# Kernel tuning notes

Hardware: AMD Instinct MI355X
Metric: run time of the kernel (lower is better)

## Reference

```python
import jax, jax.numpy as jnp
import numpy as np

D = 6            # tree depth: 63 nodes per tree, leaves-first level order
HL = 256         # lstm hidden dim
HM = 128         # mlp hid dim
OFFSETS = [0, 32, 48, 56, 60, 62]  # level l occupies [off, off+2**(D-1-l))


def _lin(k, fan_in, fan_out, scale=0.02):
    return jax.random.normal(k, (fan_in, fan_out), jnp.float32) * scale


def setup_inputs() -> dict:
    key = jax.random.key(0)
    ks = jax.random.split(key, 40)
    B, N = 1024, 63
    inp = {
        "op": jax.random.normal(ks[0], (B, N, 32), jnp.float32),
        "feat": jax.random.normal(ks[1], (B, N, 64), jnp.float32),
        "cond1": jax.random.normal(ks[2], (B, N, 256), jnp.float32),
        "cond2": jax.random.normal(ks[3], (B, N, 256), jnp.float32),
        "bitmap": jax.random.uniform(ks[4], (B, N, 1000), jnp.float32),
        "has_cond": jnp.ones((B, N), jnp.float32),
        # embeddings (stored [in, out], i.e. transposed torch Linear weight)
        "W_op": _lin(ks[5], 32, HM), "b_op": jnp.zeros((HM,), jnp.float32),
        "W_feat": _lin(ks[6], 64, HM), "b_feat": jnp.zeros((HM,), jnp.float32),
        "W_pred": _lin(ks[7], 256, HM), "b_pred": jnp.zeros((HM,), jnp.float32),
        "W_bm": _lin(ks[8], 1000, HM), "b_bm": jnp.zeros((HM,), jnp.float32),
        # node LSTM (torch layout: [4*HL, in])
        "W_ih": jax.random.normal(ks[9], (4 * HL, 5 * HM), jnp.float32) * 0.02,
        "b_ih": jnp.zeros((4 * HL,), jnp.float32),
        "W_hh": jax.random.normal(ks[10], (4 * HL, HL), jnp.float32) * 0.02,
        "b_hh": jnp.zeros((4 * HL,), jnp.float32),
        # descendant attention
        "W_wh": _lin(ks[11], HL, 64), "W_ext": _lin(ks[12], 5 * HM, 64),
        "W_a": _lin(ks[13], 64, 1),
        "W_ht": _lin(ks[14], HL, HL), "b_ht": jnp.zeros((HL,), jnp.float32),
        # output heads
        "W_c1": _lin(ks[15], HL, HM), "b_c1": jnp.zeros((HM,), jnp.float32),
        "W_c2": _lin(ks[16], HM, HM), "b_c2": jnp.zeros((HM,), jnp.float32),
        "W_c3": _lin(ks[17], HM, 1), "b_c3": jnp.zeros((1,), jnp.float32),
        "W_d1": _lin(ks[18], HL, HM), "b_d1": jnp.zeros((HM,), jnp.float32),
        "W_d2": _lin(ks[19], HM, HM), "b_d2": jnp.zeros((HM,), jnp.float32),
        "W_d3": _lin(ks[20], HM, 1), "b_d3": jnp.zeros((1,), jnp.float32),
    }
    return inp


def _tree_forward(op, feat, cond1, cond2, bitmap, has_cond,
                  W_op, b_op, W_feat, b_feat, W_pred, b_pred, W_bm, b_bm,
                  W_ih, b_ih, W_hh, b_hh, W_wh, W_ext, W_a, W_ht, b_ht):
    B = op.shape[0]
    # per-node 5*HM input vector (conditions are single Compare predicates)
    x = jnp.concatenate([
        op @ W_op + b_op,
        feat @ W_feat + b_feat,
        cond1 @ W_pred + b_pred,
        cond2 @ W_pred + b_pred,
        (bitmap @ W_bm + b_bm) * has_cond[..., None],
    ], axis=-1)                                        # [B, 63, 5*HM]

    hiddens, cells = [], []
    for l in range(D):
        n, off = 2 ** (D - 1 - l), OFFSETS[l]
        xl = x[:, off:off + n]                         # [B, n, 5*HM]
        if l == 0:  # leaves: no children, no descendants
            h0 = jnp.zeros((B, n, HL), x.dtype)
            c0 = h0
        else:
            # all descendant hiddens of each node, grouped per parent
            desc = jnp.concatenate(
                [hiddens[lp].reshape(B, n, 2 ** (l - lp), HL) for lp in range(l)],
                axis=2)                                # [B, n, M, HL]
            e = jnp.tanh(desc @ W_wh + (xl @ W_ext)[:, :, None, :])
            logits = (e @ W_a)[..., 0]                 # [B, n, M]
            w = jax.nn.softmax(logits, axis=-1)        # exp/sum(exp)
            pooled = jnp.einsum('bnm,bnmh->bnh', w, desc)
            h0 = jnp.tanh(pooled @ W_ht + b_ht)        # hidden_transformation
            c0 = 0.5 * cells[l - 1].reshape(B, n, 2, HL).sum(axis=2)  # avg child cells
        # single-step LSTM (torch gate order i, f, g, o)
        gates = xl @ W_ih.T + b_ih + h0 @ W_hh.T + b_hh
        i_, f_, g_, o_ = jnp.split(gates, 4, axis=-1)
        c = jax.nn.sigmoid(f_) * c0 + jax.nn.sigmoid(i_) * jnp.tanh(g_)
        h = jax.nn.sigmoid(o_) * jnp.tanh(c)
        hiddens.append(h)
        cells.append(c)
    return hiddens[-1][:, 0]                           # root hidden [B, HL]


def reference(op, feat, cond1, cond2, bitmap, has_cond,
              W_op, b_op, W_feat, b_feat, W_pred, b_pred, W_bm, b_bm,
              W_ih, b_ih, W_hh, b_hh, W_wh, W_ext, W_a, W_ht, b_ht,
              W_c1, b_c1, W_c2, b_c2, W_c3, b_c3,
              W_d1, b_d1, W_d2, b_d2, W_d3, b_d3):
    root = _tree_forward(op, feat, cond1, cond2, bitmap, has_cond,
                         W_op, b_op, W_feat, b_feat, W_pred, b_pred, W_bm, b_bm,
                         W_ih, b_ih, W_hh, b_hh, W_wh, W_ext, W_a, W_ht, b_ht)
    cost = jax.nn.sigmoid(jax.nn.relu(jax.nn.relu(root @ W_c1 + b_c1) @ W_c2 + b_c2) @ W_c3 + b_c3)
    card = jax.nn.sigmoid(jax.nn.relu(jax.nn.relu(root @ W_d1 + b_d1) @ W_d2 + b_d2) @ W_d3 + b_d3)
    return (cost, card)
```

## Files before the change

### kernel.cpp

```cpp
#include <hip/hip_runtime.h>
#include <math.h>

typedef unsigned short u16;
typedef __bf16 bf16x8 __attribute__((ext_vector_type(8)));
typedef float f32x4 __attribute__((ext_vector_type(4)));

static __device__ __forceinline__ float sigf(float x){ return 1.0f/(1.0f+expf(-x)); }
static __device__ __forceinline__ u16 f2bf(float f){
    unsigned u = __builtin_bit_cast(unsigned, f);
    unsigned r = u + 0x7FFFu + ((u >> 16) & 1u);
    return (u16)(r >> 16);
}
static __device__ __forceinline__ float b2f(u16 s){
    unsigned u = ((unsigned)s) << 16;
    return __builtin_bit_cast(float, u);
}

__global__ void prep_w(const float* __restrict__ W, u16* __restrict__ Wt,
                       int K, int N, int Kpad)
{
    int idx = blockIdx.x * 256 + threadIdx.x;
    if (idx >= N * Kpad) return;
    int n = idx / Kpad, k = idx - n * Kpad;
    Wt[idx] = (k < K) ? f2bf(W[(long)k * N + n]) : (u16)0;
}

__global__ void prep_g(const float* __restrict__ W_ih, const float* __restrict__ W_hh,
                       u16* __restrict__ Wt)
{
    int idx = blockIdx.x * 256 + threadIdx.x;
    int n = idx / 896, k = idx - n * 896;
    float v = (k < 640) ? W_ih[(long)n * 640 + k] : W_hh[(long)n * 256 + (k - 640)];
    Wt[idx] = f2bf(v);
}

template<bool AF32, int BN>
__launch_bounds__(256)
__global__ void gemm_bf16(const void* __restrict__ Aptr, const u16* __restrict__ Bt,
                          void* __restrict__ Cout, const float* __restrict__ bias,
                          const float* __restrict__ rowscale,
                          int Kreal, int Kpad, int lda, int ldc,
                          int permA, int act, int outBF16)
{
    constexpr int BM = 128, LDT = 40;
    constexpr int WM = (BN == 128) ? 2 : 4;
    constexpr int MI = BM / WM / 16;
    constexpr int NI = (BN == 128) ? 4 : 4;
    __shared__ u16 As[BM * LDT];
    __shared__ u16 Bs[BN * LDT];

    const int tid = threadIdx.x;
    const int lane = tid & 63, wv = tid >> 6;
    const int r0 = blockIdx.x * BM, c0 = blockIdx.y * BN;
    const int wr = (wv % WM) * (BM / WM);
    const int wc = (wv / WM) * 64;
    const int l15 = lane & 15, q8 = (lane >> 4) * 8;

    f32x4 acc[MI][NI];
#pragma unroll
    for (int i = 0; i < MI; i++)
#pragma unroll
        for (int j = 0; j < NI; j++) acc[i][j] = (f32x4){0.f, 0.f, 0.f, 0.f};

    for (int kt = 0; kt < Kpad; kt += 32) {
        if (AF32) {
            const float* Ag = (const float*)Aptr;
#pragma unroll
            for (int p = 0; p < 4; p++) {
                int v = tid + p * 256;
                int row = v >> 3, kc = (v & 7) * 4;
                long ar = r0 + row;
                long arow = permA ? ((ar & 1023) * 63 + (ar >> 10)) : ar;
                int k = kt + kc;
                float4 val;
                if (k + 4 <= Kreal) {
                    val = *(const float4*)(Ag + arow * (long)lda + k);
                } else {
                    val.x = (k + 0 < Kreal) ? Ag[arow * (long)lda + k + 0] : 0.f;
                    val.y = (k + 1 < Kreal) ? Ag[arow * (long)lda + k + 1] : 0.f;
                    val.z = (k + 2 < Kreal) ? Ag[arow * (long)lda + k + 2] : 0.f;
                    val.w = (k + 3 < Kreal) ? Ag[arow * (long)lda + k + 3] : 0.f;
                }
                ushort4 o; o.x = f2bf(val.x); o.y = f2bf(val.y); o.z = f2bf(val.z); o.w = f2bf(val.w);
                *(ushort4*)&As[row * LDT + kc] = o;
            }
        } else {
            const u16* Ag = (const u16*)Aptr;
#pragma unroll
            for (int p = 0; p < 2; p++) {
                int v = tid + p * 256;
                int row = v >> 2, kc = (v & 3) * 8;
                long ar = r0 + row;
                *(int4*)&As[row * LDT + kc] = *(const int4*)(Ag + ar * (long)lda + kt + kc);
            }
        }
        constexpr int BCH = BN * 4 / 256;
#pragma unroll
        for (int p = 0; p < BCH; p++) {
            int v = tid + p * 256;
            int row = v >> 2, kc = (v & 3) * 8;
            *(int4*)&Bs[row * LDT + kc] = *(const int4*)(Bt + (long)(c0 + row) * Kpad + kt + kc);
        }
        __syncthreads();

        bf16x8 af[MI], bfr[NI];
#pragma unroll
        for (int mi = 0; mi < MI; mi++)
            af[mi] = *reinterpret_cast<const bf16x8*>(&As[(wr + mi * 16 + l15) * LDT + q8]);
#pragma unroll
        for (int ni = 0; ni < NI; ni++)
            bfr[ni] = *reinterpret_cast<const bf16x8*>(&Bs[(wc + ni * 16 + l15) * LDT + q8]);
#pragma unroll
        for (int mi = 0; mi < MI; mi++)
#pragma unroll
            for (int ni = 0; ni < NI; ni++)
                acc[mi][ni] = __builtin_amdgcn_mfma_f32_16x16x32_bf16(af[mi], bfr[ni], acc[mi][ni], 0, 0, 0);
        __syncthreads();
    }

#pragma unroll
    for (int mi = 0; mi < MI; mi++) {
#pragma unroll
        for (int ni = 0; ni < NI; ni++) {
#pragma unroll
            for (int r = 0; r < 4; r++) {
                int row = r0 + wr + mi * 16 + (lane >> 4) * 4 + r;
                int col = c0 + wc + ni * 16 + l15;
                float v = acc[mi][ni][r];
                if (bias) v += bias[col];
                if (act == 1) v = tanhf(v);
                if (rowscale) v *= rowscale[(row & 1023) * 63 + (row >> 10)];
                if (outBF16) ((u16*)Cout)[(long)row * ldc + col] = f2bf(v);
                else         ((float*)Cout)[(long)row * ldc + col] = v;
            }
        }
    }
}

__launch_bounds__(256)
__global__ void gates_mfma(const u16* __restrict__ xl, const u16* __restrict__ h0,
                           const u16* __restrict__ Wt_g,
                           const float* __restrict__ b_ih, const float* __restrict__ b_hh,
                           const float* __restrict__ Cprev,
                           u16* __restrict__ Hbuf, float* __restrict__ Cbuf,
                           int offCur, int offPrev, int Ktot)
{
    constexpr int LDT = 40;
    __shared__ u16 smem[128 * 136];
    __shared__ float bias_s[4][32];
    u16* As = smem;
    u16* Bs = smem + 128 * LDT;
    u16* Gs = smem;

    const int tid = threadIdx.x;
    const int lane = tid & 63, wv = tid >> 6;
    const int r0 = blockIdx.x * 128;
    const int by32 = blockIdx.y * 32;
    const int wr = (wv & 1) * 64, wc = (wv >> 1) * 64;
    const int l15 = lane & 15, q8 = (lane >> 4) * 8;

    if (tid < 128) {
        int g = tid >> 5, c = tid & 31;
        int gcol = g * 256 + by32 + c;
        bias_s[g][c] = b_ih[gcol] + b_hh[gcol];
    }

    f32x4 acc[4][4];
#pragma unroll
    for (int i = 0; i < 4; i++)
#pragma unroll
        for (int j = 0; j < 4; j++) acc[i][j] = (f32x4){0.f, 0.f, 0.f, 0.f};

    for (int kt = 0; kt < Ktot; kt += 32) {
#pragma unroll
        for (int p = 0; p < 2; p++) {
            int v = tid + p * 256;
            int row = v >> 2, kc = (v & 3) * 8;
            long ar = r0 + row;
            int k = kt + kc;
            int4 val;
            if (k < 640) val = *(const int4*)(xl + ar * 640L + k);
            else         val = *(const int4*)(h0 + ar * 256L + (k - 640));
            *(int4*)&As[row * LDT + kc] = val;
        }
#pragma unroll
        for (int p = 0; p < 2; p++) {
            int v = tid + p * 256;
            int row = v >> 2, kc = (v & 3) * 8;
            long brow = (long)((row >> 5) * 256 + by32 + (row & 31));
            *(int4*)&Bs[row * LDT + kc] = *(const int4*)(Wt_g + brow * 896 + kt + kc);
        }
        __syncthreads();

        bf16x8 af[4], bfr[4];
#pragma unroll
        for (int mi = 0; mi < 4; mi++)
            af[mi] = *reinterpret_cast<const bf16x8*>(&As[(wr + mi * 16 + l15) * LDT + q8]);
#pragma unroll
        for (int ni = 0; ni < 4; ni++)
            bfr[ni] = *reinterpret_cast<const bf16x8*>(&Bs[(wc + ni * 16 + l15) * LDT + q8]);
#pragma unroll
        for (int mi = 0; mi < 4; mi++)
#pragma unroll
            for (int ni = 0; ni < 4; ni++)
                acc[mi][ni] = __builtin_amdgcn_mfma_f32_16x16x32_bf16(af[mi], bfr[ni], acc[mi][ni], 0, 0, 0);
        __syncthreads();
    }

#pragma unroll
    for (int mi = 0; mi < 4; mi++)
#pragma unroll
        for (int ni = 0; ni < 4; ni++)
#pragma unroll
            for (int r = 0; r < 4; r++) {
                int lr = wr + mi * 16 + (lane >> 4) * 4 + r;
                int lc = wc + ni * 16 + l15;
                Gs[lr * 136 + lc] = f2bf(acc[mi][ni][r]);
            }
    __syncthreads();

#pragma unroll
    for (int i = 0; i < 16; i++) {
        int r = (tid >> 5) * 16 + i;
        int c = tid & 31;
        float iv = b2f(Gs[r * 136 + c])      + bias_s[0][c];
        float fv = b2f(Gs[r * 136 + 32 + c]) + bias_s[1][c];
        float gv = b2f(Gs[r * 136 + 64 + c]) + bias_s[2][c];
        float ov = b2f(Gs[r * 136 + 96 + c]) + bias_s[3][c];
        int rloc = r0 + r;
        int nd = rloc >> 10, bb = rloc & 1023;
        int gcol = by32 + c;
        float c0v = 0.f;
        if (Cprev) {
            long ch = ((long)(offPrev + nd * 2) * 1024 + bb) * 256 + gcol;
            c0v = 0.5f * (Cprev[ch] + Cprev[ch + 262144]);
        }
        float cv = sigf(fv) * c0v + sigf(iv) * tanhf(gv);
        float hv = sigf(ov) * tanhf(cv);
        long orow = ((long)offCur * 1024 + rloc) * 256 + gcol;
        Cbuf[orow] = cv;
        Hbuf[orow] = f2bf(hv);
    }
}

__launch_bounds__(256)
__global__ void attn_logits(const float* __restrict__ E, const float* __restrict__ xextall,
                            const float* __restrict__ W_a, float* __restrict__ Lbuf,
                            int level, int rows, int m, int off)
{
    const int wv = threadIdx.x >> 6, ln = threadIdx.x & 63;
    const long dr = (long)blockIdx.x * 4 + wv;
    if (dr >= rows) return;
    const int g = (int)(dr >> 10), bb = (int)(dr & 1023);
    int lp, node;
    if      (g < 32) { lp = 0; node = g;      }
    else if (g < 48) { lp = 1; node = g - 32; }
    else if (g < 56) { lp = 2; node = g - 48; }
    else if (g < 60) { lp = 3; node = g - 56; }
    else             { lp = 4; node = g - 60; }
    const int shift  = level - lp;
    const int i      = node >> shift;
    const int within = node & ((1 << shift) - 1);
    const int d      = ((2 << level) - (2 << shift)) + within;

    float e = E[dr * 64 + ln] + xextall[((long)(off + i) * 1024 + bb) * 64 + ln];
    float v = tanhf(e) * W_a[ln];
#pragma unroll
    for (int s = 32; s; s >>= 1) v += __shfl_xor(v, s);
    if (ln == 0) Lbuf[((long)(i * m + d)) * 1024 + bb] = v;
}

__launch_bounds__(256)
__global__ void attn_pool(const float* __restrict__ Lbuf, const u16* __restrict__ Hbuf,
                          float* __restrict__ pooled, int level, int m)
{
    const int blk = blockIdx.x;
    const int i = blk >> 10, bb = blk & 1023;
    const int tid = threadIdx.x;
    __shared__ float raw[64];
    __shared__ float wsm[64];
    if (tid < m) raw[tid] = Lbuf[((long)(i * m + tid)) * 1024 + bb];
    __syncthreads();
    if (tid == 0) {
        float mx = -1e30f;
        for (int d = 0; d < m; d++) mx = fmaxf(mx, raw[d]);
        float s = 0.f;
        for (int d = 0; d < m; d++) { float e = expf(raw[d] - mx); wsm[d] = e; s += e; }
        float inv = 1.f / s;
        for (int d = 0; d < m; d++) wsm[d] *= inv;
    }
    __syncthreads();
    float accv = 0.f;
    const int h = tid;
    int cum = 0;
    for (int lp = 0; lp < level; lp++) {
        int sz = 1 << (level - lp);
        int base = 64 - (64 >> lp);
        for (int q = 0; q < sz; q++) {
            long row = (long)(base + i * sz + q) * 1024 + bb;
            accv = fmaf(wsm[cum + q], b2f(Hbuf[row * 256 + h]), accv);
        }
        cum += sz;
    }
    pooled[(long)blk * 256 + h] = accv;
}

__launch_bounds__(256)
__global__ void heads_kernel(const u16* __restrict__ Hbuf,
                             const float* __restrict__ W_c1, const float* __restrict__ b_c1,
                             const float* __restrict__ W_c2, const float* __restrict__ b_c2,
                             const float* __restrict__ W_c3, const float* __restrict__ b_c3,
                             const float* __restrict__ W_d1, const float* __restrict__ b_d1,
                             const float* __restrict__ W_d2, const float* __restrict__ b_d2,
                             const float* __restrict__ W_d3, const float* __restrict__ b_d3,
                             float* __restrict__ out)
{
    const int bb = blockIdx.x, tid = threadIdx.x;
    __shared__ float root[256];
    __shared__ float t1[128];
    __shared__ float t2[128];
    __shared__ float red[256];
    root[tid] = b2f(Hbuf[((long)62 * 1024 + bb) * 256 + tid]);
    __syncthreads();
    for (int head = 0; head < 2; head++) {
        const float* w1  = head ? W_d1 : W_c1;
        const float* bi1 = head ? b_d1 : b_c1;
        const float* w2  = head ? W_d2 : W_c2;
        const float* bi2 = head ? b_d2 : b_c2;
        const float* w3  = head ? W_d3 : W_c3;
        const float* bi3 = head ? b_d3 : b_c3;
        if (tid < 128) {
            float s = bi1[tid];
            for (int k = 0; k < 256; k++) s = fmaf(root[k], w1[k * 128 + tid], s);
            t1[tid] = fmaxf(s, 0.f);
        }
        __syncthreads();
        if (tid < 128) {
            float s = bi2[tid];
            for (int k = 0; k < 128; k++) s = fmaf(t1[k], w2[k * 128 + tid], s);
            t2[tid] = fmaxf(s, 0.f);
        }
        __syncthreads();
        red[tid] = (tid < 128) ? t2[tid] * w3[tid] : 0.f;
        __syncthreads();
        for (int s = 128; s; s >>= 1) { if (tid < s) red[tid] += red[tid + s]; __syncthreads(); }
        if (tid == 0) out[head * 1024 + bb] = sigf(red[0] + bi3[0]);
        __syncthreads();
    }
}

extern "C" void kernel_launch(void* const* d_in, const int* in_sizes, int n_in,
                              void* d_out, int out_size, void* d_ws, size_t ws_size,
                              hipStream_t stream)
{
    (void)in_sizes; (void)n_in; (void)out_size;
    const float* op       = (const float*)d_in[0];
    const float* feat     = (const float*)d_in[1];
    const float* cond1    = (const float*)d_in[2];
    const float* cond2    = (const float*)d_in[3];
    const float* bitmap   = (const float*)d_in[4];
    const float* has_cond = (const float*)d_in[5];
    const float* W_op     = (const float*)d_in[6];
    const float* b_op     = (const float*)d_in[7];
    const float* W_feat   = (const float*)d_in[8];
    const float* b_feat   = (const float*)d_in[9];
    const float* W_pred   = (const float*)d_in[10];
    const float* b_pred   = (const float*)d_in[11];
    const float* W_bm     = (const float*)d_in[12];
    const float* b_bm     = (const float*)d_in[13];
    const float* W_ih     = (const float*)d_in[14];
    const float* b_ih     = (const float*)d_in[15];
    const float* W_hh     = (const float*)d_in[16];
    const float* b_hh     = (const float*)d_in[17];
    const float* W_wh     = (const float*)d_in[18];
    const float* W_ext    = (const float*)d_in[19];
    const float* W_a      = (const float*)d_in[20];
    const float* W_ht     = (const float*)d_in[21];
    const float* b_ht     = (const float*)d_in[22];
    const float* W_c1     = (const float*)d_in[23];
    const float* b_c1     = (const float*)d_in[24];
    const float* W_c2     = (const float*)d_in[25];
    const float* b_c2     = (const float*)d_in[26];
    const float* W_c3     = (const float*)d_in[27];
    const float* b_c3     = (const float*)d_in[28];
    const float* W_d1     = (const float*)d_in[29];
    const float* b_d1     = (const float*)d_in[30];
    const float* W_d2     = (const float*)d_in[31];
    const float* b_d2     = (const float*)d_in[32];
    const float* W_d3     = (const float*)d_in[33];
    const float* b_d3     = (const float*)d_in[34];
    float* out = (float*)d_out;

    char* p = (char*)d_ws;
    auto alloc = [&](size_t bytes) -> char* {
        char* r = p; p += (bytes + 255) & ~(size_t)255; return r;
    };
    u16*   xall    = (u16*)  alloc((size_t)64512 * 640 * 2);
    float* xextall = (float*)alloc((size_t)64512 * 64 * 4);
    u16*   Hbuf    = (u16*)  alloc((size_t)64512 * 256 * 2);
    float* Cbuf    = (float*)alloc((size_t)64512 * 256 * 4);
    float* Ebuf    = (float*)alloc((size_t)62 * 1024 * 64 * 4);
    float* pooled  = (float*)alloc((size_t)16384 * 256 * 4);
    u16*   h0      = (u16*)  alloc((size_t)16384 * 256 * 2);
    float* Lbuf    = (float*)alloc((size_t)65536 * 4);
    u16*   Wt_op   = (u16*)  alloc((size_t)128 * 32 * 2);
    u16*   Wt_feat = (u16*)  alloc((size_t)128 * 64 * 2);
    u16*   Wt_pred = (u16*)  alloc((size_t)128 * 256 * 2);
    u16*   Wt_bm   = (u16*)  alloc((size_t)128 * 1024 * 2);
    u16*   Wt_g    = (u16*)  alloc((size_t)1024 * 896 * 2);
    u16*   Wt_wh   = (u16*)  alloc((size_t)64 * 256 * 2);
    u16*   Wt_ext  = (u16*)  alloc((size_t)64 * 640 * 2);
    u16*   Wt_ht   = (u16*)  alloc((size_t)256 * 256 * 2);
    if (ws_size < (size_t)(p - (char*)d_ws)) return;

    prep_w<<<16,  256, 0, stream>>>(W_op,   Wt_op,   32,   128, 32);
    prep_w<<<32,  256, 0, stream>>>(W_feat, Wt_feat, 64,   128, 64);
    prep_w<<<128, 256, 0, stream>>>(W_pred, Wt_pred, 256,  128, 256);
    prep_w<<<512, 256, 0, stream>>>(W_bm,   Wt_bm,   1000, 128, 1024);
    prep_w<<<64,  256, 0, stream>>>(W_wh,   Wt_wh,   256,  64,  256);
    prep_w<<<160, 256, 0, stream>>>(W_ext,  Wt_ext,  640,  64,  640);
    prep_w<<<256, 256, 0, stream>>>(W_ht,   Wt_ht,   256,  256, 256);
    prep_g<<<3584,256, 0, stream>>>(W_ih, W_hh, Wt_g);

    gemm_bf16<true,128><<<dim3(504,1), 256, 0, stream>>>(op,     Wt_op,   (void*)(xall + 0),   b_op,   nullptr,  32,   32,   32,   640, 1, 0, 1);
    gemm_bf16<true,128><<<dim3(504,1), 256, 0, stream>>>(feat,   Wt_feat, (void*)(xall + 128), b_feat, nullptr,  64,   64,   64,   640, 1, 0, 1);
    gemm_bf16<true,128><<<dim3(504,1), 256, 0, stream>>>(cond1,  Wt_pred, (void*)(xall + 256), b_pred, nullptr,  256,  256,  256,  640, 1, 0, 1);
    gemm_bf16<true,128><<<dim3(504,1), 256, 0, stream>>>(cond2,  Wt_pred, (void*)(xall + 384), b_pred, nullptr,  256,  256,  256,  640, 1, 0, 1);
    gemm_bf16<true,128><<<dim3(504,1), 256, 0, stream>>>(bitmap, Wt_bm,   (void*)(xall + 512), b_bm,   has_cond, 1000, 1024, 1000, 640, 1, 0, 1);
    gemm_bf16<false,64><<<dim3(504,1), 256, 0, stream>>>(xall, Wt_ext, (void*)xextall, nullptr, nullptr, 640, 640, 640, 64, 0, 0, 0);

    for (int l = 0; l < 6; l++) {
        const int n   = 32 >> l;
        const int off = 64 - (64 >> l);
        const int M   = n * 1024;
        const int m   = (2 << l) - 2;

        if (l > 0) {
            int rows = off * 1024;
            attn_logits<<<rows / 4, 256, 0, stream>>>(Ebuf, xextall, W_a, Lbuf, l, rows, m, off);
            attn_pool<<<M, 256, 0, stream>>>(Lbuf, Hbuf, pooled, l, m);
            gemm_bf16<true,128><<<dim3(M/128, 2), 256, 0, stream>>>(pooled, Wt_ht, (void*)h0, b_ht, nullptr, 256, 256, 256, 256, 0, 1, 1);
        }

        const int Ktot    = l ? 896 : 640;
        const int offPrev = l ? (64 - (64 >> (l - 1))) : 0;
        gates_mfma<<<dim3(M/128, 8), 256, 0, stream>>>(xall + (size_t)off * 1024 * 640, h0, Wt_g,
                                                       b_ih, b_hh, l ? Cbuf : nullptr,
                                                       Hbuf, Cbuf, off, offPrev, Ktot);

        if (l < 5) {
            gemm_bf16<false,64><<<dim3(M/128, 1), 256, 0, stream>>>(Hbuf + (size_t)off * 1024 * 256, Wt_wh,
                                                                    (void*)(Ebuf + (size_t)off * 1024 * 64),
                                                                    nullptr, nullptr, 256, 256, 256, 64, 0, 0, 0);
        }
    }

    heads_kernel<<<1024, 256, 0, stream>>>(Hbuf, W_c1, b_c1, W_c2, b_c2, W_c3, b_c3,
                                           W_d1, b_d1, W_d2, b_d2, W_d3, b_d3, out);
}
```

Measured before the change: 1.392 ms.

## Precompute input-gate projections for all nodes in one GEMM, recurrent kernel only does h·W_hh

Hoists the x·W_ih product for all 63 levels of nodes into a single large bf16 GEMM (with the summed biases folded in) that writes a bf16 gate-preactivation buffer. Level 0 becomes a pure elementwise LSTM kernel, and later levels run a smaller K=256 recurrent GEMM that adds the precomputed x-gates in its epilogue, with wider per-block tiles covering all four gates for 64 cells. The cost being removed is launching many smaller per-level GEMMs with K=896 over the same shared weights. In exchange it adds a 64512x1024 bf16 intermediate that is written once and read back, plus an extra rounding of the x-part to bf16.

```diff
diff --git a/kernel.cpp b/kernel.cpp
--- a/kernel.cpp
+++ b/kernel.cpp
@@ -24,14 +24,16 @@
     int n = idx / Kpad, k = idx - n * Kpad;
     Wt[idx] = (k < K) ? f2bf(W[(long)k * N + n]) : (u16)0;
 }
-
-__global__ void prep_g(const float* __restrict__ W_ih, const float* __restrict__ W_hh,
-                       u16* __restrict__ Wt)
+__global__ void prep_cvt(const float* __restrict__ W, u16* __restrict__ Wt, int total)
 {
     int idx = blockIdx.x * 256 + threadIdx.x;
-    int n = idx / 896, k = idx - n * 896;
-    float v = (k < 640) ? W_ih[(long)n * 640 + k] : W_hh[(long)n * 256 + (k - 640)];
-    Wt[idx] = f2bf(v);
+    if (idx < total) Wt[idx] = f2bf(W[idx]);
+}
+__global__ void prep_bias(const float* __restrict__ b_ih, const float* __restrict__ b_hh,
+                          float* __restrict__ bsum)
+{
+    int idx = blockIdx.x * 256 + threadIdx.x;
+    if (idx < 1024) bsum[idx] = b_ih[idx] + b_hh[idx];
 }
 
 template<bool AF32, int BN>
@@ -43,9 +45,10 @@
                           int permA, int act, int outBF16)
 {
     constexpr int BM = 128, LDT = 40;
-    constexpr int WM = (BN == 128) ? 2 : 4;
+    constexpr int WM = (BN >= 128) ? 2 : 4;
+    constexpr int WN = 4 / WM;
     constexpr int MI = BM / WM / 16;
-    constexpr int NI = (BN == 128) ? 4 : 4;
+    constexpr int NI = BN / WN / 16;
     __shared__ u16 As[BM * LDT];
     __shared__ u16 Bs[BN * LDT];
 
@@ -53,7 +56,7 @@
     const int lane = tid & 63, wv = tid >> 6;
     const int r0 = blockIdx.x * BM, c0 = blockIdx.y * BN;
     const int wr = (wv % WM) * (BM / WM);
-    const int wc = (wv / WM) * 64;
+    const int wc = (wv / WM) * (BN / WN);
     const int l15 = lane & 15, q8 = (lane >> 4) * 8;
 
     f32x4 acc[MI][NI];
@@ -138,16 +141,40 @@
 }
 
 __launch_bounds__(256)
-__global__ void gates_mfma(const u16* __restrict__ xl, const u16* __restrict__ h0,
-                           const u16* __restrict__ Wt_g,
-                           const float* __restrict__ b_ih, const float* __restrict__ b_hh,
-                           const float* __restrict__ Cprev,
-                           u16* __restrict__ Hbuf, float* __restrict__ Cbuf,
-                           int offCur, int offPrev, int Ktot)
-{
-    constexpr int LDT = 40;
-    __shared__ u16 smem[128 * 136];
-    __shared__ float bias_s[4][32];
+__global__ void lstm0(const u16* __restrict__ xg, u16* __restrict__ Hbuf,
+                      float* __restrict__ Cbuf)
+{
+    int idx = blockIdx.x * 256 + threadIdx.x;
+    int row = idx >> 6;
+    int c4 = (idx & 63) * 4;
+    const u16* g = xg + (long)row * 1024;
+    ushort4 i4 = *(const ushort4*)(g + c4);
+    ushort4 g4 = *(const ushort4*)(g + 512 + c4);
+    ushort4 o4 = *(const ushort4*)(g + 768 + c4);
+    float cv[4], hv[4];
+    u16 iv[4] = {i4.x, i4.y, i4.z, i4.w};
+    u16 gv[4] = {g4.x, g4.y, g4.z, g4.w};
+    u16 ov[4] = {o4.x, o4.y, o4.z, o4.w};
+#pragma unroll
+    for (int j = 0; j < 4; j++) {
+        cv[j] = sigf(b2f(iv[j])) * tanhf(b2f(gv[j]));
+        hv[j] = sigf(b2f(ov[j])) * tanhf(cv[j]);
+    }
+    long ob = (long)row * 256 + c4;
+    *(float4*)(Cbuf + ob) = make_float4(cv[0], cv[1], cv[2], cv[3]);
+    ushort4 h4; h4.x = f2bf(hv[0]); h4.y = f2bf(hv[1]); h4.z = f2bf(hv[2]); h4.w = f2bf(hv[3]);
+    *(ushort4*)(Hbuf + ob) = h4;
+}
+
+__launch_bounds__(256)
+__global__ void gates_h(const u16* __restrict__ h0, const u16* __restrict__ Wt_hh,
+                        const u16* __restrict__ xg,
+                        const float* __restrict__ Cprev,
+                        u16* __restrict__ Hbuf, float* __restrict__ Cbuf,
+                        int offCur, int offPrev)
+{
+    constexpr int LDT = 40, LDG = 264;
+    __shared__ u16 smem[128 * LDG];
     u16* As = smem;
     u16* Bs = smem + 128 * LDT;
     u16* Gs = smem;
@@ -155,54 +182,43 @@
     const int tid = threadIdx.x;
     const int lane = tid & 63, wv = tid >> 6;
     const int r0 = blockIdx.x * 128;
-    const int by32 = blockIdx.y * 32;
-    const int wr = (wv & 1) * 64, wc = (wv >> 1) * 64;
+    const int cb = blockIdx.y * 64;
+    const int wr = (wv & 1) * 64, wc = (wv >> 1) * 128;
     const int l15 = lane & 15, q8 = (lane >> 4) * 8;
 
-    if (tid < 128) {
-        int g = tid >> 5, c = tid & 31;
-        int gcol = g * 256 + by32 + c;
-        bias_s[g][c] = b_ih[gcol] + b_hh[gcol];
-    }
-
-    f32x4 acc[4][4];
+    f32x4 acc[4][8];
 #pragma unroll
     for (int i = 0; i < 4; i++)
 #pragma unroll
-        for (int j = 0; j < 4; j++) acc[i][j] = (f32x4){0.f, 0.f, 0.f, 0.f};
-
-    for (int kt = 0; kt < Ktot; kt += 32) {
+        for (int j = 0; j < 8; j++) acc[i][j] = (f32x4){0.f, 0.f, 0.f, 0.f};
+
+    for (int kt = 0; kt < 256; kt += 32) {
 #pragma unroll
         for (int p = 0; p < 2; p++) {
             int v = tid + p * 256;
             int row = v >> 2, kc = (v & 3) * 8;
-            long ar = r0 + row;
-            int k = kt + kc;
-            int4 val;
-            if (k < 640) val = *(const int4*)(xl + ar * 640L + k);
-            else         val = *(const int4*)(h0 + ar * 256L + (k - 640));
-            *(int4*)&As[row * LDT + kc] = val;
-        }
-#pragma unroll
-        for (int p = 0; p < 2; p++) {
+            *(int4*)&As[row * LDT + kc] = *(const int4*)(h0 + (long)(r0 + row) * 256 + kt + kc);
+        }
+#pragma unroll
+        for (int p = 0; p < 4; p++) {
             int v = tid + p * 256;
             int row = v >> 2, kc = (v & 3) * 8;
-            long brow = (long)((row >> 5) * 256 + by32 + (row & 31));
-            *(int4*)&Bs[row * LDT + kc] = *(const int4*)(Wt_g + brow * 896 + kt + kc);
-        }
-        __syncthreads();
-
-        bf16x8 af[4], bfr[4];
+            long brow = (long)((row >> 6) * 256 + cb + (row & 63));
+            *(int4*)&Bs[row * LDT + kc] = *(const int4*)(Wt_hh + brow * 256 + kt + kc);
+        }
+        __syncthreads();
+
+        bf16x8 af[4], bfr[8];
 #pragma unroll
         for (int mi = 0; mi < 4; mi++)
             af[mi] = *reinterpret_cast<const bf16x8*>(&As[(wr + mi * 16 + l15) * LDT + q8]);
 #pragma unroll
-        for (int ni = 0; ni < 4; ni++)
+        for (int ni = 0; ni < 8; ni++)
             bfr[ni] = *reinterpret_cast<const bf16x8*>(&Bs[(wc + ni * 16 + l15) * LDT + q8]);
 #pragma unroll
         for (int mi = 0; mi < 4; mi++)
 #pragma unroll
-            for (int ni = 0; ni < 4; ni++)
+            for (int ni = 0; ni < 8; ni++)
                 acc[mi][ni] = __builtin_amdgcn_mfma_f32_16x16x32_bf16(af[mi], bfr[ni], acc[mi][ni], 0, 0, 0);
         __syncthreads();
     }
@@ -210,31 +226,31 @@
 #pragma unroll
     for (int mi = 0; mi < 4; mi++)
 #pragma unroll
-        for (int ni = 0; ni < 4; ni++)
+        for (int ni = 0; ni < 8; ni++)
 #pragma unroll
             for (int r = 0; r < 4; r++) {
                 int lr = wr + mi * 16 + (lane >> 4) * 4 + r;
                 int lc = wc + ni * 16 + l15;
-                Gs[lr * 136 + lc] = f2bf(acc[mi][ni][r]);
+                int gc = (lc >> 6) * 256 + cb + (lc & 63);
+                long xrow = (long)offCur * 1024 + r0 + lr;
+                float v = acc[mi][ni][r] + b2f(xg[xrow * 1024 + gc]);
+                Gs[lr * LDG + lc] = f2bf(v);
             }
     __syncthreads();
 
 #pragma unroll
-    for (int i = 0; i < 16; i++) {
-        int r = (tid >> 5) * 16 + i;
-        int c = tid & 31;
-        float iv = b2f(Gs[r * 136 + c])      + bias_s[0][c];
-        float fv = b2f(Gs[r * 136 + 32 + c]) + bias_s[1][c];
-        float gv = b2f(Gs[r * 136 + 64 + c]) + bias_s[2][c];
-        float ov = b2f(Gs[r * 136 + 96 + c]) + bias_s[3][c];
-        int rloc = r0 + r;
+    for (int i = 0; i < 32; i++) {
+        int idx = i * 256 + tid;
+        int row = idx >> 6, cell = idx & 63;
+        float iv = b2f(Gs[row * LDG + cell]);
+        float fv = b2f(Gs[row * LDG + 64 + cell]);
+        float gv = b2f(Gs[row * LDG + 128 + cell]);
+        float ov = b2f(Gs[row * LDG + 192 + cell]);
+        int rloc = r0 + row;
         int nd = rloc >> 10, bb = rloc & 1023;
-        int gcol = by32 + c;
-        float c0v = 0.f;
-        if (Cprev) {
-            long ch = ((long)(offPrev + nd * 2) * 1024 + bb) * 256 + gcol;
-            c0v = 0.5f * (Cprev[ch] + Cprev[ch + 262144]);
-        }
+        int gcol = cb + cell;
+        long ch = ((long)(offPrev + nd * 2) * 1024 + bb) * 256 + gcol;
+        float c0v = 0.5f * (Cprev[ch] + Cprev[ch + 262144]);
         float cv = sigf(fv) * c0v + sigf(iv) * tanhf(gv);
         float hv = sigf(ov) * tanhf(cv);
         long orow = ((long)offCur * 1024 + rloc) * 256 + gcol;
@@ -396,6 +412,7 @@
         char* r = p; p += (bytes + 255) & ~(size_t)255; return r;
     };
     u16*   xall    = (u16*)  alloc((size_t)64512 * 640 * 2);
+    u16*   xg      = (u16*)  alloc((size_t)64512 * 1024 * 2);
     float* xextall = (float*)alloc((size_t)64512 * 64 * 4);
     u16*   Hbuf    = (u16*)  alloc((size_t)64512 * 256 * 2);
     float* Cbuf    = (float*)alloc((size_t)64512 * 256 * 4);
@@ -407,10 +424,12 @@
     u16*   Wt_feat = (u16*)  alloc((size_t)128 * 64 * 2);
     u16*   Wt_pred = (u16*)  alloc((size_t)128 * 256 * 2);
     u16*   Wt_bm   = (u16*)  alloc((size_t)128 * 1024 * 2);
-    u16*   Wt_g    = (u16*)  alloc((size_t)1024 * 896 * 2);
+    u16*   Wt_ih   = (u16*)  alloc((size_t)1024 * 640 * 2);
+    u16*   Wt_hh   = (u16*)  alloc((size_t)1024 * 256 * 2);
     u16*   Wt_wh   = (u16*)  alloc((size_t)64 * 256 * 2);
     u16*   Wt_ext  = (u16*)  alloc((size_t)64 * 640 * 2);
     u16*   Wt_ht   = (u16*)  alloc((size_t)256 * 256 * 2);
+    float* bsum    = (float*)alloc((size_t)1024 * 4);
     if (ws_size < (size_t)(p - (char*)d_ws)) return;
 
     prep_w<<<16,  256, 0, stream>>>(W_op,   Wt_op,   32,   128, 32);
@@ -420,7 +439,9 @@
     prep_w<<<64,  256, 0, stream>>>(W_wh,   Wt_wh,   256,  64,  256);
     prep_w<<<160, 256, 0, stream>>>(W_ext,  Wt_ext,  640,  64,  640);
     prep_w<<<256, 256, 0, stream>>>(W_ht,   Wt_ht,   256,  256, 256);
-    prep_g<<<3584,256, 0, stream>>>(W_ih, W_hh, Wt_g);
+    prep_cvt<<<2560, 256, 0, stream>>>(W_ih, Wt_ih, 1024 * 640);
+    prep_cvt<<<1024, 256, 0, stream>>>(W_hh, Wt_hh, 1024 * 256);
+    prep_bias<<<4, 256, 0, stream>>>(b_ih, b_hh, bsum);
 
     gemm_bf16<true,128><<<dim3(504,1), 256, 0, stream>>>(op,     Wt_op,   (void*)(xall + 0),   b_op,   nullptr,  32,   32,   32,   640, 1, 0, 1);
     gemm_bf16<true,128><<<dim3(504,1), 256, 0, stream>>>(feat,   Wt_feat, (void*)(xall + 128), b_feat, nullptr,  64,   64,   64,   640, 1, 0, 1);
@@ -428,6 +449,7 @@
     gemm_bf16<true,128><<<dim3(504,1), 256, 0, stream>>>(cond2,  Wt_pred, (void*)(xall + 384), b_pred, nullptr,  256,  256,  256,  640, 1, 0, 1);
     gemm_bf16<true,128><<<dim3(504,1), 256, 0, stream>>>(bitmap, Wt_bm,   (void*)(xall + 512), b_bm,   has_cond, 1000, 1024, 1000, 640, 1, 0, 1);
     gemm_bf16<false,64><<<dim3(504,1), 256, 0, stream>>>(xall, Wt_ext, (void*)xextall, nullptr, nullptr, 640, 640, 640, 64, 0, 0, 0);
+    gemm_bf16<false,256><<<dim3(504,4), 256, 0, stream>>>(xall, Wt_ih, (void*)xg, bsum, nullptr, 640, 640, 640, 1024, 0, 0, 1);
 
     for (int l = 0; l < 6; l++) {
         const int n   = 32 >> l;
@@ -440,13 +462,11 @@
             attn_logits<<<rows / 4, 256, 0, stream>>>(Ebuf, xextall, W_a, Lbuf, l, rows, m, off);
             attn_pool<<<M, 256, 0, stream>>>(Lbuf, Hbuf, pooled, l, m);
             gemm_bf16<true,128><<<dim3(M/128, 2), 256, 0, stream>>>(pooled, Wt_ht, (void*)h0, b_ht, nullptr, 256, 256, 256, 256, 0, 1, 1);
-        }
-
-        const int Ktot    = l ? 896 : 640;
-        const int offPrev = l ? (64 - (64 >> (l - 1))) : 0;
-        gates_mfma<<<dim3(M/128, 8), 256, 0, stream>>>(xall + (size_t)off * 1024 * 640, h0, Wt_g,
-                                                       b_ih, b_hh, l ? Cbuf : nullptr,
-                                                       Hbuf, Cbuf, off, offPrev, Ktot);
+            const int offPrev = 64 - (64 >> (l - 1));
+            gates_h<<<dim3(M/128, 4), 256, 0, stream>>>(h0, Wt_hh, xg, Cbuf, Hbuf, Cbuf, off, offPrev);
+        } else {
+            lstm0<<<8192, 256, 0, stream>>>(xg, Hbuf, Cbuf);
+        }
 
         if (l < 5) {
             gemm_bf16<false,64><<<dim3(M/128, 1), 256, 0, stream>>>(Hbuf + (size_t)off * 1024 * 256, Wt_wh,
```

After: 1.693 ms. +21.6%, slower.
